# Kernel tuning notes

Measured on AMD Instinct MI355X. Metric: run time of the kernel, lower is better.

Reference implementation:

```python
import jax, jax.numpy as jnp
import numpy as np


def build_perm(total_channels, num_filters):
    """Replicates Net.permuted_new_perfect's nested slice-copies as one gather index."""
    ncpf = total_channels // num_filters
    tg = num_filters + ncpf * ((num_filters - 1) * num_filters) // 2
    perm = np.zeros(tg * ncpf, dtype=np.int32)
    count = 0
    for i in range(num_filters):
        for j in range(ncpf):
            if j == 0:
                for k in range(i, num_filters):
                    perm[count] = i * ncpf
                    perm[count + 1:count + ncpf] = np.arange(k * ncpf + 1, k * ncpf + ncpf)
                    count += ncpf
            else:
                for k in range(i + 1, num_filters):
                    perm[count + j] = i * ncpf + j
                    perm[count:count + j] = np.arange(k * ncpf, k * ncpf + j)
                    perm[count + j + 1:count + ncpf] = np.arange(k * ncpf + j + 1, k * ncpf + ncpf)
                    count += ncpf
    return jnp.asarray(perm)


PERM1 = build_perm(18, 6)    # 153 gathered channels, 51 groups of 3
PERM2 = build_perm(255, 5)   # 26265 gathered channels, 515 groups of 51


def dw_conv(x, w, b, groups):
    y = jax.lax.conv_general_dilated(
        x, w, window_strides=(1, 1), padding='VALID',
        dimension_numbers=('NCHW', 'OIHW', 'NCHW'),
        feature_group_count=groups)
    return y + b[None, :, None, None]


def maxpool2(x):
    return jax.lax.reduce_window(x, -jnp.inf, jax.lax.max,
                                 (1, 1, 2, 2), (1, 1, 2, 2), 'VALID')


def perm_groupconv(x, perm, w, b):
    # gather channels, then grouped 1x1 conv (each group: ncpf chans -> 1 chan)
    G, ncpf = w.shape
    B, _, H, W = x.shape
    xg = x[:, perm].reshape(B, G, ncpf, H, W)
    return jnp.einsum('bgchw,gc->bghw', xg, w) + b[None, :, None, None]


def setup_inputs() -> dict:
    key = jax.random.key(0)
    ks = jax.random.split(key, 17)
    s = 0.05
    return {
        'x': jax.random.normal(ks[0], (64, 3, 32, 32), jnp.float32),
        'dw1_w': jax.random.normal(ks[1], (18, 1, 5, 5), jnp.float32) * s,
        'dw1_b': jax.random.normal(ks[2], (18,), jnp.float32) * s,
        'pc1_w': jax.random.normal(ks[3], (51, 3), jnp.float32) * s,
        'pc1_b': jax.random.normal(ks[4], (51,), jnp.float32) * s,
        'dw2_w': jax.random.normal(ks[5], (255, 1, 5, 5), jnp.float32) * s,
        'dw2_b': jax.random.normal(ks[6], (255,), jnp.float32) * s,
        'pc2_w': jax.random.normal(ks[7], (515, 51), jnp.float32) * s,
        'pc2_b': jax.random.normal(ks[8], (515,), jnp.float32) * s,
        'oo_w': jax.random.normal(ks[9], (100, 515), jnp.float32) * s,
        'oo_b': jax.random.normal(ks[10], (100,), jnp.float32) * s,
        'fc1_w': jax.random.normal(ks[11], (120, 2500), jnp.float32) * s,
        'fc1_b': jax.random.normal(ks[12], (120,), jnp.float32) * s,
        'fc2_w': jax.random.normal(ks[13], (84, 120), jnp.float32) * s,
        'fc2_b': jax.random.normal(ks[14], (84,), jnp.float32) * s,
        'fc3_w': jax.random.normal(ks[15], (10, 84), jnp.float32) * s,
        'fc3_b': jax.random.normal(ks[16], (10,), jnp.float32) * s,
    }


def reference(x, dw1_w, dw1_b, pc1_w, pc1_b, dw2_w, dw2_b, pc2_w, pc2_b,
              oo_w, oo_b, fc1_w, fc1_b, fc2_w, fc2_b, fc3_w, fc3_b):
    h = dw_conv(x, dw1_w, dw1_b, groups=3)            # [B,18,28,28]
    h = perm_groupconv(h, PERM1, pc1_w, pc1_b)        # [B,51,28,28]
    h = maxpool2(jax.nn.relu(h))                      # [B,51,14,14]
    h = dw_conv(h, dw2_w, dw2_b, groups=51)           # [B,255,10,10]
    h = perm_groupconv(h, PERM2, pc2_w, pc2_b)        # [B,515,10,10]
    h = maxpool2(jax.nn.relu(h))                      # [B,515,5,5]
    h = jax.nn.relu(jnp.einsum('bchw,oc->bohw', h, oo_w) + oo_b[None, :, None, None])  # [B,100,5,5]
    h = h.reshape(h.shape[0], -1)                     # [B,2500]
    h = jax.nn.relu(h @ fc1_w.T + fc1_b)
    h = jax.nn.relu(h @ fc2_w.T + fc2_b)
    return h @ fc3_w.T + fc3_b                        # [B,10]
```

## Files before the change

kernel.cpp:

```cpp
#include <hip/hip_runtime.h>

static constexpr size_t OFF_XT = 0;
static constexpr size_t OFF_H1 = 786432;
static constexpr size_t OFF_H2 = 4399104;
static constexpr size_t OFF_H3 = 6958080;
static constexpr size_t OFF_H4 = 13486080;
static constexpr size_t OFF_H5 = 16782080;
static constexpr size_t OFF_H5B = OFF_H1;
static constexpr size_t OFF_H6 = 17422080;
static constexpr size_t OFF_H7 = 17452800;
static constexpr size_t OFF_M1 = 17474304;
static constexpr size_t OFF_M2 = 17475328;
static constexpr size_t OFF_W2 = 17484032;

struct Meta2 { int g; int special; float wj; int valid; };

__device__ inline void scan_ijk(int F, int ncpf, int g, int& oi, int& oj, int& ok) {
  int cnt = 0;
  for (int i = 0; i < F; ++i)
    for (int j = 0; j < ncpf; ++j) {
      int ks = (j == 0) ? i : i + 1;
      for (int k = ks; k < F; ++k) {
        if (cnt == g) { oi = i; oj = j; ok = k; return; }
        ++cnt;
      }
    }
  oi = 0; oj = 0; ok = 0;
}

__device__ inline float4 f4fma(float4 v, float w, float4 a) {
  a.x = fmaf(v.x, w, a.x); a.y = fmaf(v.y, w, a.y);
  a.z = fmaf(v.z, w, a.z); a.w = fmaf(v.w, w, a.w);
  return a;
}

__global__ void k0_setup(const float* __restrict__ x, const float* __restrict__ pc2_w,
                         float* ws) {
  int bx = blockIdx.x, tid = threadIdx.x;
  if (bx < 96) {
    __shared__ float t[64][33];
    int c = bx >> 5, y = bx & 31;
    for (int r = 0; r < 8; ++r) {
      int b = r * 8 + (tid >> 5), xx = tid & 31;
      t[b][xx] = x[((b * 3 + c) * 32 + y) * 32 + xx];
    }
    __syncthreads();
    float* xT = ws + OFF_XT / 4;
    for (int r = 0; r < 8; ++r) {
      int xx = r * 4 + (tid >> 6), b = tid & 63;
      xT[((c * 32 + y) * 32 + xx) * 64 + b] = t[b][xx];
    }
  } else if (bx == 96) {
    if (tid < 51) {
      int i, j, k; scan_ijk(6, 3, tid, i, j, k);
      int* src1 = (int*)((char*)ws + OFF_M1);
      for (int p = 0; p < 3; ++p)
        src1[tid * 4 + p] = (p == j) ? (i * 3 + j) : (k * 3 + p);
    }
  } else if (bx < 204) {
    int idx = (bx - 97) * 256 + tid;
    if (idx < 536 * 51) {
      int s = idx / 51, p = idx - s * 51;
      int k, base;
      if (s < 8)        { k = 0; base = 0; }
      else if (s < 64)  { k = 1; base = 8; }
      else if (s < 168) { k = 2; base = 64; }
      else if (s < 328) { k = 3; base = 168; }
      else              { k = 4; base = 328; }
      int id2 = s - base;
      int cnt = 51 * k + 1;
      Meta2* m2 = (Meta2*)((char*)ws + OFF_M2);
      float* W2 = (float*)((char*)ws + OFF_W2);
      if (id2 < cnt) {
        int i, j;
        if (id2 <= k) { i = id2; j = 0; }
        else { int t2 = id2 - (k + 1); i = t2 / 50; j = t2 - i * 50 + 1; }
        int off = 205 * i - 51 * ((i * (i - 1)) >> 1);
        int g = (j == 0) ? (off + (k - i))
                         : (off + (5 - i) + (j - 1) * (4 - i) + (k - i - 1));
        W2[s * 51 + p] = (p == j) ? 0.f : pc2_w[g * 51 + p];
        if (p == 0) {
          m2[s].g = g; m2[s].special = i * 51 + j;
          m2[s].wj = pc2_w[g * 51 + j]; m2[s].valid = 1;
        }
      } else {
        W2[s * 51 + p] = 0.f;
        if (p == 0) { m2[s].g = 0; m2[s].special = 0; m2[s].wj = 0.f; m2[s].valid = 0; }
      }
    }
  } else {
    int idx = (bx - 204) * 256 + tid;
    if (idx < 7680) (ws + OFF_H6 / 4)[idx] = 0.f;
  }
}

__global__ void __launch_bounds__(256) k1_dw1(const float* __restrict__ w,
                                              const float* __restrict__ bias, float* ws) {
  const float* xT = ws + OFF_XT / 4;
  float* h1 = ws + OFF_H1 / 4;
  int task = blockIdx.x * 4 + __builtin_amdgcn_readfirstlane(threadIdx.y);
  int l = threadIdx.x;
  int sub = l >> 4, b4 = (l & 15) * 4;
  int o = task / 196, rem = task - o * 196;
  int y = rem / 7, xo = (rem - y * 7) * 4 + sub;
  int c = o / 6;
  float bb = bias[o];
  float4 acc = {bb, bb, bb, bb};
  const float* src = xT + ((c * 32 + y) * 32 + xo) * 64 + b4;
  #pragma unroll
  for (int ky = 0; ky < 5; ++ky)
    #pragma unroll
    for (int kx = 0; kx < 5; ++kx) {
      float4 v = *(const float4*)(src + (ky * 32 + kx) * 64);
      acc = f4fma(v, w[o * 25 + ky * 5 + kx], acc);
    }
  *(float4*)(h1 + ((o * 28 + y) * 28 + xo) * 64 + b4) = acc;
}

__global__ void __launch_bounds__(256) k2_pc1(const float* __restrict__ w,
                                              const float* __restrict__ bias, float* ws) {
  const float* h1 = ws + OFF_H1 / 4;
  const int* src1 = (const int*)((const char*)ws + OFF_M1);
  float* h2 = ws + OFF_H2 / 4;
  int task = blockIdx.x * 4 + __builtin_amdgcn_readfirstlane(threadIdx.y);
  if (task >= 2499) return;
  int l = threadIdx.x;
  int sub = l >> 4, b4 = (l & 15) * 4;
  int g = task / 49, pc = task - g * 49;
  int pp = pc * 4 + sub;
  int py = pp / 14, px = pp - py * 14;
  int s0 = src1[g * 4 + 0], s1 = src1[g * 4 + 1], s2 = src1[g * 4 + 2];
  float w0 = w[g * 3 + 0], w1 = w[g * 3 + 1], w2 = w[g * 3 + 2], bb = bias[g];
  float4 m = {0.f, 0.f, 0.f, 0.f};
  #pragma unroll
  for (int dy = 0; dy < 2; ++dy)
    #pragma unroll
    for (int dx = 0; dx < 2; ++dx) {
      int y = py * 2 + dy, xx = px * 2 + dx;
      float4 a = {bb, bb, bb, bb};
      a = f4fma(*(const float4*)(h1 + ((s0 * 28 + y) * 28 + xx) * 64 + b4), w0, a);
      a = f4fma(*(const float4*)(h1 + ((s1 * 28 + y) * 28 + xx) * 64 + b4), w1, a);
      a = f4fma(*(const float4*)(h1 + ((s2 * 28 + y) * 28 + xx) * 64 + b4), w2, a);
      m.x = fmaxf(m.x, a.x); m.y = fmaxf(m.y, a.y);
      m.z = fmaxf(m.z, a.z); m.w = fmaxf(m.w, a.w);
    }
  *(float4*)(h2 + ((g * 14 + py) * 14 + px) * 64 + b4) = m;
}

__global__ void __launch_bounds__(256) k3_dw2(const float* __restrict__ w,
                                              const float* __restrict__ bias, float* ws) {
  const float* h2 = ws + OFF_H2 / 4;
  float* h3 = ws + OFF_H3 / 4;
  int task = blockIdx.x * 4 + __builtin_amdgcn_readfirstlane(threadIdx.y);
  if (task >= 6375) return;
  int l = threadIdx.x;
  int sub = l >> 4, b4 = (l & 15) * 4;
  int o = task / 25, pc = task - o * 25;
  int p = pc * 4 + sub;
  int y = p / 10, xo = p - y * 10;
  int c = o / 5;
  float bb = bias[o];
  float4 acc = {bb, bb, bb, bb};
  const float* src = h2 + ((c * 14 + y) * 14 + xo) * 64 + b4;
  #pragma unroll
  for (int ky = 0; ky < 5; ++ky)
    #pragma unroll
    for (int kx = 0; kx < 5; ++kx) {
      float4 v = *(const float4*)(src + (ky * 14 + kx) * 64);
      acc = f4fma(v, w[o * 25 + ky * 5 + kx], acc);
    }
  int py = y >> 1, dy = y & 1, px = xo >> 1, dx = xo & 1;
  *(float4*)(h3 + ((o * 25 + py * 5 + px) * 4 + dy * 2 + dx) * 64 + b4) = acc;
}

__global__ void __launch_bounds__(256) k4_pc2(const float* __restrict__ bias, float* ws) {
  const float* h3 = ws + OFF_H3 / 4;
  const float* W2 = (const float*)((const char*)ws + OFF_W2);
  const Meta2* m2 = (const Meta2*)((const char*)ws + OFF_M2);
  float* h4 = ws + OFF_H4 / 4;
  int b = threadIdx.x;
  int wv = __builtin_amdgcn_readfirstlane(threadIdx.y);
  int pyx = blockIdx.x;
  int chunk = blockIdx.y;
  int k;
  if (chunk < 1) k = 0; else if (chunk < 8) k = 1; else if (chunk < 21) k = 2;
  else if (chunk < 41) k = 3; else k = 4;
  int s0 = chunk * 8 + wv * 2;
  float acc[2][4];
  #pragma unroll
  for (int m = 0; m < 2; ++m)
    #pragma unroll
    for (int q = 0; q < 4; ++q) acc[m][q] = 0.f;
  const float* hb = h3 + (size_t)(k * 51 * 100 + pyx * 4) * 64 + b;
  const float* wr0 = W2 + (s0 + 0) * 51;
  const float* wr1 = W2 + (s0 + 1) * 51;
  for (int p = 0; p < 51; ++p) {
    float v0 = hb[p * 6400 + 0];
    float v1 = hb[p * 6400 + 64];
    float v2 = hb[p * 6400 + 128];
    float v3 = hb[p * 6400 + 192];
    float wa = wr0[p], wb = wr1[p];
    acc[0][0] = fmaf(v0, wa, acc[0][0]);
    acc[0][1] = fmaf(v1, wa, acc[0][1]);
    acc[0][2] = fmaf(v2, wa, acc[0][2]);
    acc[0][3] = fmaf(v3, wa, acc[0][3]);
    acc[1][0] = fmaf(v0, wb, acc[1][0]);
    acc[1][1] = fmaf(v1, wb, acc[1][1]);
    acc[1][2] = fmaf(v2, wb, acc[1][2]);
    acc[1][3] = fmaf(v3, wb, acc[1][3]);
  }
  #pragma unroll
  for (int m = 0; m < 2; ++m) {
    Meta2 mm = m2[s0 + m];
    if (!mm.valid) continue;
    const float* hs = h3 + (size_t)(mm.special * 100 + pyx * 4) * 64 + b;
    float bb = bias[mm.g];
    float r0 = fmaf(hs[0],   mm.wj, acc[m][0]) + bb;
    float r1 = fmaf(hs[64],  mm.wj, acc[m][1]) + bb;
    float r2 = fmaf(hs[128], mm.wj, acc[m][2]) + bb;
    float r3 = fmaf(hs[192], mm.wj, acc[m][3]) + bb;
    float r = fmaxf(fmaxf(r0, r1), fmaxf(r2, r3));
    h4[(mm.g * 25 + pyx) * 64 + b] = fmaxf(r, 0.f);
  }
}

__global__ void __launch_bounds__(256) k5_oo(const float* __restrict__ w, float* ws) {
  const float* h4 = ws + OFF_H4 / 4;
  __shared__ float red[4][4][64];
  int lane = threadIdx.x;
  int wv = __builtin_amdgcn_readfirstlane(threadIdx.y);
  int pyx = blockIdx.x, og = blockIdx.y, ks = blockIdx.z;
  int kb = ks ? 258 : 0;
  int kn = ks ? 257 : 258;
  int q = kn >> 2, r = kn & 3;
  int base = __builtin_amdgcn_readfirstlane(kb + wv * q + (wv < r ? wv : r));
  int n = q + (wv < r ? 1 : 0);
  const float* w0 = w + (og * 4 + 0) * 515;
  const float* w1 = w + (og * 4 + 1) * 515;
  const float* w2 = w + (og * 4 + 2) * 515;
  const float* w3 = w + (og * 4 + 3) * 515;
  const float* hp = h4 + pyx * 64 + lane;
  float a0 = 0.f, a1 = 0.f, a2 = 0.f, a3 = 0.f;
  #pragma unroll 4
  for (int i = 0; i < n; ++i) {
    int c = base + i;
    float v = hp[c * 1600];
    a0 = fmaf(v, w0[c], a0);
    a1 = fmaf(v, w1[c], a1);
    a2 = fmaf(v, w2[c], a2);
    a3 = fmaf(v, w3[c], a3);
  }
  red[wv][0][lane] = a0; red[wv][1][lane] = a1;
  red[wv][2][lane] = a2; red[wv][3][lane] = a3;
  __syncthreads();
  if (wv == 0) {
    float* h5p = ws + (ks ? OFF_H5B : OFF_H5) / 4;
    #pragma unroll
    for (int m = 0; m < 4; ++m) {
      float s = red[0][m][lane] + red[1][m][lane] + red[2][m][lane] + red[3][m][lane];
      h5p[((og * 4 + m) * 25 + pyx) * 64 + lane] = s;
    }
  }
}

__global__ void __launch_bounds__(256) k6_fc1(const float* __restrict__ w,
                                              const float* __restrict__ oo_b, float* ws) {
  const float* h5a = ws + OFF_H5 / 4;
  const float* h5b = ws + OFF_H5B / 4;
  float* h6 = ws + OFF_H6 / 4;
  __shared__ float red[4][4][64];
  int lane = threadIdx.x;
  int wv = __builtin_amdgcn_readfirstlane(threadIdx.y);
  int og = blockIdx.x, ks = blockIdx.y;
  int kb = ks * 156 + (ks < 4 ? ks : 4);
  int kn = 156 + (ks < 4 ? 1 : 0);
  int q = kn >> 2, r = kn & 3;
  int base = __builtin_amdgcn_readfirstlane(kb + wv * q + (wv < r ? wv : r));
  int n = q + (wv < r ? 1 : 0);
  const float* w0 = w + (og * 4 + 0) * 2500;
  const float* w1 = w + (og * 4 + 1) * 2500;
  const float* w2 = w + (og * 4 + 2) * 2500;
  const float* w3 = w + (og * 4 + 3) * 2500;
  float a0 = 0.f, a1 = 0.f, a2 = 0.f, a3 = 0.f;
  #pragma unroll 4
  for (int i = 0; i < n; ++i) {
    int k = base + i;
    float v = fmaxf(h5a[k * 64 + lane] + h5b[k * 64 + lane] + oo_b[k / 25], 0.f);
    a0 = fmaf(v, w0[k], a0);
    a1 = fmaf(v, w1[k], a1);
    a2 = fmaf(v, w2[k], a2);
    a3 = fmaf(v, w3[k], a3);
  }
  red[wv][0][lane] = a0; red[wv][1][lane] = a1;
  red[wv][2][lane] = a2; red[wv][3][lane] = a3;
  __syncthreads();
  if (wv == 0) {
    #pragma unroll
    for (int m = 0; m < 4; ++m) {
      float s = red[0][m][lane] + red[1][m][lane] + red[2][m][lane] + red[3][m][lane];
      atomicAdd(&h6[(og * 4 + m) * 64 + lane], s);
    }
  }
}

__global__ void __launch_bounds__(256) k7_fc2(const float* __restrict__ w,
                                              const float* __restrict__ fc1_b,
                                              const float* __restrict__ bias, float* ws) {
  const float* h6 = ws + OFF_H6 / 4;
  float* h7 = ws + OFF_H7 / 4;
  __shared__ float red[4][64];
  int lane = threadIdx.x & 63, wv = threadIdx.x >> 6;
  int o = blockIdx.x;
  float acc = 0.f;
  int i0 = wv * 30;
  #pragma unroll 5
  for (int i = i0; i < i0 + 30; ++i) {
    float v = fmaxf(h6[i * 64 + lane] + fc1_b[i], 0.f);
    acc = fmaf(v, w[o * 120 + i], acc);
  }
  red[wv][lane] = acc;
  __syncthreads();
  if (threadIdx.x < 64) {
    float s = red[0][lane] + red[1][lane] + red[2][lane] + red[3][lane] + bias[o];
    h7[o * 64 + lane] = fmaxf(s, 0.f);
  }
}

__global__ void __launch_bounds__(256) k8_fc3(const float* __restrict__ w,
                                              const float* __restrict__ bias,
                                              float* out, const float* ws) {
  const float* h7 = ws + OFF_H7 / 4;
  __shared__ float red[4][64];
  int lane = threadIdx.x & 63, wv = threadIdx.x >> 6;
  int o = blockIdx.x;
  float acc = 0.f;
  int i0 = wv * 21;
  #pragma unroll 7
  for (int i = i0; i < i0 + 21; ++i)
    acc = fmaf(h7[i * 64 + lane], w[o * 84 + i], acc);
  red[wv][lane] = acc;
  __syncthreads();
  if (threadIdx.x < 64) {
    float s = red[0][lane] + red[1][lane] + red[2][lane] + red[3][lane] + bias[o];
    out[lane * 10 + o] = s;
  }
}

extern "C" void kernel_launch(void* const* d_in, const int* in_sizes, int n_in,
                              void* d_out, int out_size, void* d_ws, size_t ws_size,
                              hipStream_t stream) {
  const float* x     = (const float*)d_in[0];
  const float* dw1_w = (const float*)d_in[1];
  const float* dw1_b = (const float*)d_in[2];
  const float* pc1_w = (const float*)d_in[3];
  const float* pc1_b = (const float*)d_in[4];
  const float* dw2_w = (const float*)d_in[5];
  const float* dw2_b = (const float*)d_in[6];
  const float* pc2_w = (const float*)d_in[7];
  const float* pc2_b = (const float*)d_in[8];
  const float* oo_w  = (const float*)d_in[9];
  const float* oo_b  = (const float*)d_in[10];
  const float* fc1_w = (const float*)d_in[11];
  const float* fc1_b = (const float*)d_in[12];
  const float* fc2_w = (const float*)d_in[13];
  const float* fc2_b = (const float*)d_in[14];
  const float* fc3_w = (const float*)d_in[15];
  const float* fc3_b = (const float*)d_in[16];
  float* ws = (float*)d_ws;
  float* out = (float*)d_out;

  hipLaunchKernelGGL(k0_setup, dim3(234), dim3(256), 0, stream, x, pc2_w, ws);
  hipLaunchKernelGGL(k1_dw1, dim3(882), dim3(64, 4), 0, stream, dw1_w, dw1_b, ws);
  hipLaunchKernelGGL(k2_pc1, dim3(625), dim3(64, 4), 0, stream, pc1_w, pc1_b, ws);
  hipLaunchKernelGGL(k3_dw2, dim3(1594), dim3(64, 4), 0, stream, dw2_w, dw2_b, ws);
  hipLaunchKernelGGL(k4_pc2, dim3(25, 67), dim3(64, 4), 0, stream, pc2_b, ws);
  hipLaunchKernelGGL(k5_oo, dim3(25, 25, 2), dim3(64, 4), 0, stream, oo_w, ws);
  hipLaunchKernelGGL(k6_fc1, dim3(30, 16), dim3(64, 4), 0, stream, fc1_w, oo_b, ws);
  hipLaunchKernelGGL(k7_fc2, dim3(84), dim3(256), 0, stream, fc2_w, fc1_b, fc2_b, ws);
  hipLaunchKernelGGL(k8_fc3, dim3(10), dim3(256), 0, stream, fc3_w, fc3_b, out, ws);
}
```

Measured before the change: 150.2 us.

## Fuse 1x1 conv and three FC layers into one per-sample tail kernel

Replaces the oo, fc1, fc2 and fc3 kernels with a single kernel that runs one block per batch sample. Each block stages its slice of h4 in LDS and computes all remaining layers there. This removes three launches, the h5/h6/h7 round-trips through global memory, the atomics and the zeroing of h6 in setup. The cost is only 64 blocks, one per sample, each re-reading the full oo and fc1 weights serially, so parallelism drops sharply.

```diff
diff --git a/kernel.cpp b/kernel.cpp
--- a/kernel.cpp
+++ b/kernel.cpp
@@ -5,10 +5,6 @@
 static constexpr size_t OFF_H2 = 4399104;
 static constexpr size_t OFF_H3 = 6958080;
 static constexpr size_t OFF_H4 = 13486080;
-static constexpr size_t OFF_H5 = 16782080;
-static constexpr size_t OFF_H5B = OFF_H1;
-static constexpr size_t OFF_H6 = 17422080;
-static constexpr size_t OFF_H7 = 17452800;
 static constexpr size_t OFF_M1 = 17474304;
 static constexpr size_t OFF_M2 = 17475328;
 static constexpr size_t OFF_W2 = 17484032;
@@ -57,7 +53,7 @@
       for (int p = 0; p < 3; ++p)
         src1[tid * 4 + p] = (p == j) ? (i * 3 + j) : (k * 3 + p);
     }
-  } else if (bx < 204) {
+  } else {
     int idx = (bx - 97) * 256 + tid;
     if (idx < 536 * 51) {
       int s = idx / 51, p = idx - s * 51;
@@ -88,9 +84,6 @@
         if (p == 0) { m2[s].g = 0; m2[s].special = 0; m2[s].wj = 0.f; m2[s].valid = 0; }
       }
     }
-  } else {
-    int idx = (bx - 204) * 256 + tid;
-    if (idx < 7680) (ws + OFF_H6 / 4)[idx] = 0.f;
   }
 }
 
@@ -224,125 +217,91 @@
   }
 }
 
-__global__ void __launch_bounds__(256) k5_oo(const float* __restrict__ w, float* ws) {
+static constexpr int TL_H4 = 0;
+static constexpr int TL_OL = 12880;
+static constexpr int TL_H6 = 15380;
+static constexpr int TL_H7 = 15504;
+static constexpr int TL_PART = 0;
+
+__global__ void __launch_bounds__(256) k_tail(const float* __restrict__ oo_w,
+                                              const float* __restrict__ oo_b,
+                                              const float* __restrict__ fc1_w,
+                                              const float* __restrict__ fc1_b,
+                                              const float* __restrict__ fc2_w,
+                                              const float* __restrict__ fc2_b,
+                                              const float* __restrict__ fc3_w,
+                                              const float* __restrict__ fc3_b,
+                                              float* out, const float* ws) {
+  __shared__ float lds[16384];
   const float* h4 = ws + OFF_H4 / 4;
-  __shared__ float red[4][4][64];
-  int lane = threadIdx.x;
-  int wv = __builtin_amdgcn_readfirstlane(threadIdx.y);
-  int pyx = blockIdx.x, og = blockIdx.y, ks = blockIdx.z;
-  int kb = ks ? 258 : 0;
-  int kn = ks ? 257 : 258;
-  int q = kn >> 2, r = kn & 3;
-  int base = __builtin_amdgcn_readfirstlane(kb + wv * q + (wv < r ? wv : r));
-  int n = q + (wv < r ? 1 : 0);
-  const float* w0 = w + (og * 4 + 0) * 515;
-  const float* w1 = w + (og * 4 + 1) * 515;
-  const float* w2 = w + (og * 4 + 2) * 515;
-  const float* w3 = w + (og * 4 + 3) * 515;
-  const float* hp = h4 + pyx * 64 + lane;
-  float a0 = 0.f, a1 = 0.f, a2 = 0.f, a3 = 0.f;
-  #pragma unroll 4
-  for (int i = 0; i < n; ++i) {
-    int c = base + i;
-    float v = hp[c * 1600];
-    a0 = fmaf(v, w0[c], a0);
-    a1 = fmaf(v, w1[c], a1);
-    a2 = fmaf(v, w2[c], a2);
-    a3 = fmaf(v, w3[c], a3);
-  }
-  red[wv][0][lane] = a0; red[wv][1][lane] = a1;
-  red[wv][2][lane] = a2; red[wv][3][lane] = a3;
-  __syncthreads();
-  if (wv == 0) {
-    float* h5p = ws + (ks ? OFF_H5B : OFF_H5) / 4;
-    #pragma unroll
-    for (int m = 0; m < 4; ++m) {
-      float s = red[0][m][lane] + red[1][m][lane] + red[2][m][lane] + red[3][m][lane];
-      h5p[((og * 4 + m) * 25 + pyx) * 64 + lane] = s;
-    }
-  }
-}
-
-__global__ void __launch_bounds__(256) k6_fc1(const float* __restrict__ w,
-                                              const float* __restrict__ oo_b, float* ws) {
-  const float* h5a = ws + OFF_H5 / 4;
-  const float* h5b = ws + OFF_H5B / 4;
-  float* h6 = ws + OFF_H6 / 4;
-  __shared__ float red[4][4][64];
-  int lane = threadIdx.x;
-  int wv = __builtin_amdgcn_readfirstlane(threadIdx.y);
-  int og = blockIdx.x, ks = blockIdx.y;
-  int kb = ks * 156 + (ks < 4 ? ks : 4);
-  int kn = 156 + (ks < 4 ? 1 : 0);
-  int q = kn >> 2, r = kn & 3;
-  int base = __builtin_amdgcn_readfirstlane(kb + wv * q + (wv < r ? wv : r));
-  int n = q + (wv < r ? 1 : 0);
-  const float* w0 = w + (og * 4 + 0) * 2500;
-  const float* w1 = w + (og * 4 + 1) * 2500;
-  const float* w2 = w + (og * 4 + 2) * 2500;
-  const float* w3 = w + (og * 4 + 3) * 2500;
-  float a0 = 0.f, a1 = 0.f, a2 = 0.f, a3 = 0.f;
-  #pragma unroll 4
-  for (int i = 0; i < n; ++i) {
-    int k = base + i;
-    float v = fmaxf(h5a[k * 64 + lane] + h5b[k * 64 + lane] + oo_b[k / 25], 0.f);
-    a0 = fmaf(v, w0[k], a0);
-    a1 = fmaf(v, w1[k], a1);
-    a2 = fmaf(v, w2[k], a2);
-    a3 = fmaf(v, w3[k], a3);
-  }
-  red[wv][0][lane] = a0; red[wv][1][lane] = a1;
-  red[wv][2][lane] = a2; red[wv][3][lane] = a3;
-  __syncthreads();
-  if (wv == 0) {
-    #pragma unroll
-    for (int m = 0; m < 4; ++m) {
-      float s = red[0][m][lane] + red[1][m][lane] + red[2][m][lane] + red[3][m][lane];
-      atomicAdd(&h6[(og * 4 + m) * 64 + lane], s);
-    }
-  }
-}
-
-__global__ void __launch_bounds__(256) k7_fc2(const float* __restrict__ w,
-                                              const float* __restrict__ fc1_b,
-                                              const float* __restrict__ bias, float* ws) {
-  const float* h6 = ws + OFF_H6 / 4;
-  float* h7 = ws + OFF_H7 / 4;
-  __shared__ float red[4][64];
-  int lane = threadIdx.x & 63, wv = threadIdx.x >> 6;
-  int o = blockIdx.x;
-  float acc = 0.f;
-  int i0 = wv * 30;
-  #pragma unroll 5
-  for (int i = i0; i < i0 + 30; ++i) {
-    float v = fmaxf(h6[i * 64 + lane] + fc1_b[i], 0.f);
-    acc = fmaf(v, w[o * 120 + i], acc);
-  }
-  red[wv][lane] = acc;
-  __syncthreads();
-  if (threadIdx.x < 64) {
-    float s = red[0][lane] + red[1][lane] + red[2][lane] + red[3][lane] + bias[o];
-    h7[o * 64 + lane] = fmaxf(s, 0.f);
-  }
-}
-
-__global__ void __launch_bounds__(256) k8_fc3(const float* __restrict__ w,
-                                              const float* __restrict__ bias,
-                                              float* out, const float* ws) {
-  const float* h7 = ws + OFF_H7 / 4;
-  __shared__ float red[4][64];
-  int lane = threadIdx.x & 63, wv = threadIdx.x >> 6;
-  int o = blockIdx.x;
-  float acc = 0.f;
-  int i0 = wv * 21;
-  #pragma unroll 7
-  for (int i = i0; i < i0 + 21; ++i)
-    acc = fmaf(h7[i * 64 + lane], w[o * 84 + i], acc);
-  red[wv][lane] = acc;
-  __syncthreads();
-  if (threadIdx.x < 64) {
-    float s = red[0][lane] + red[1][lane] + red[2][lane] + red[3][lane] + bias[o];
-    out[lane * 10 + o] = s;
+  const int b = blockIdx.x;
+  const int t = threadIdx.x;
+
+  for (int i = t; i < 12875; i += 256)
+    lds[TL_H4 + i] = h4[i * 64 + b];
+  __syncthreads();
+
+  if (t < 250) {
+    int pyx = t % 25, og = t / 25;
+    float acc[10];
+    #pragma unroll
+    for (int j = 0; j < 10; ++j) acc[j] = 0.f;
+    const float* wb = oo_w + og * 10 * 515;
+    for (int c = 0; c < 515; ++c) {
+      float v = lds[TL_H4 + c * 25 + pyx];
+      #pragma unroll
+      for (int j = 0; j < 10; ++j)
+        acc[j] = fmaf(v, wb[j * 515 + c], acc[j]);
+    }
+    #pragma unroll
+    for (int j = 0; j < 10; ++j) {
+      int o = og * 10 + j;
+      lds[TL_OL + o * 25 + pyx] = fmaxf(acc[j] + oo_b[o], 0.f);
+    }
+  }
+  __syncthreads();
+
+  if (t < 240) {
+    int og = t / 20, kc = t % 20;
+    float acc[10];
+    #pragma unroll
+    for (int j = 0; j < 10; ++j) acc[j] = 0.f;
+    int kbase = kc * 125;
+    const float* wb = fc1_w + og * 10 * 2500 + kbase;
+    for (int i = 0; i < 125; ++i) {
+      float v = lds[TL_OL + kbase + i];
+      #pragma unroll
+      for (int j = 0; j < 10; ++j)
+        acc[j] = fmaf(v, wb[j * 2500 + i], acc[j]);
+    }
+    #pragma unroll
+    for (int j = 0; j < 10; ++j)
+      lds[TL_PART + (og * 10 + j) * 20 + kc] = acc[j];
+  }
+  __syncthreads();
+  if (t < 120) {
+    float s = fc1_b[t];
+    #pragma unroll
+    for (int kc = 0; kc < 20; ++kc) s += lds[TL_PART + t * 20 + kc];
+    lds[TL_H6 + t] = fmaxf(s, 0.f);
+  }
+  __syncthreads();
+
+  if (t < 84) {
+    float s = fc2_b[t];
+    #pragma unroll 8
+    for (int i = 0; i < 120; ++i)
+      s = fmaf(lds[TL_H6 + i], fc2_w[t * 120 + i], s);
+    lds[TL_H7 + t] = fmaxf(s, 0.f);
+  }
+  __syncthreads();
+
+  if (t < 10) {
+    float s = fc3_b[t];
+    #pragma unroll 7
+    for (int i = 0; i < 84; ++i)
+      s = fmaf(lds[TL_H7 + i], fc3_w[t * 84 + i], s);
+    out[b * 10 + t] = s;
   }
 }
 
@@ -369,13 +328,11 @@
   float* ws = (float*)d_ws;
   float* out = (float*)d_out;
 
-  hipLaunchKernelGGL(k0_setup, dim3(234), dim3(256), 0, stream, x, pc2_w, ws);
+  hipLaunchKernelGGL(k0_setup, dim3(204), dim3(256), 0, stream, x, pc2_w, ws);
   hipLaunchKernelGGL(k1_dw1, dim3(882), dim3(64, 4), 0, stream, dw1_w, dw1_b, ws);
   hipLaunchKernelGGL(k2_pc1, dim3(625), dim3(64, 4), 0, stream, pc1_w, pc1_b, ws);
   hipLaunchKernelGGL(k3_dw2, dim3(1594), dim3(64, 4), 0, stream, dw2_w, dw2_b, ws);
   hipLaunchKernelGGL(k4_pc2, dim3(25, 67), dim3(64, 4), 0, stream, pc2_b, ws);
-  hipLaunchKernelGGL(k5_oo, dim3(25, 25, 2), dim3(64, 4), 0, stream, oo_w, ws);
-  hipLaunchKernelGGL(k6_fc1, dim3(30, 16), dim3(64, 4), 0, stream, fc1_w, oo_b, ws);
-  hipLaunchKernelGGL(k7_fc2, dim3(84), dim3(256), 0, stream, fc2_w, fc1_b, fc2_b, ws);
-  hipLaunchKernelGGL(k8_fc3, dim3(10), dim3(256), 0, stream, fc3_w, fc3_b, out, ws);
-}
+  hipLaunchKernelGGL(k_tail, dim3(64), dim3(256), 0, stream,
+                     oo_w, oo_b, fc1_w, fc1_b, fc2_w, fc2_b, fc3_w, fc3_b, out, ws);
+}
```

Measured after the change: 472.5 us. 215% more time.

## Fuse fc2 and fc3 into one per-sample kernel; widen pc2 register tile

Applied to the files above, without the earlier changes.

Merges the separate fc2 and fc3 kernels into a single kernel with one block per sample, keeping the 120- and 84-wide activations in shared memory, which removes one launch and the global round-trip of h7. Separately, each wave in pc2 now computes four output groups instead of two, so each loaded activation is reused across more weights, and the grid shrinks to about half with per-wave k/s0 mapping and early exit for padding waves. The trade-off is fewer blocks and more registers in pc2, and poorly coalesced per-thread weight-row reads in the fused FC kernel.

```diff
diff --git a/kernel.cpp b/kernel.cpp
--- a/kernel.cpp
+++ b/kernel.cpp
@@ -8,7 +8,6 @@
 static constexpr size_t OFF_H5 = 16782080;
 static constexpr size_t OFF_H5B = OFF_H1;
 static constexpr size_t OFF_H6 = 17422080;
-static constexpr size_t OFF_H7 = 17452800;
 static constexpr size_t OFF_M1 = 17474304;
 static constexpr size_t OFF_M2 = 17475328;
 static constexpr size_t OFF_W2 = 17484032;
@@ -181,25 +180,30 @@
   int b = threadIdx.x;
   int wv = __builtin_amdgcn_readfirstlane(threadIdx.y);
   int pyx = blockIdx.x;
-  int chunk = blockIdx.y;
-  int k;
-  if (chunk < 1) k = 0; else if (chunk < 8) k = 1; else if (chunk < 21) k = 2;
-  else if (chunk < 41) k = 3; else k = 4;
-  int s0 = chunk * 8 + wv * 2;
-  float acc[2][4];
-  #pragma unroll
-  for (int m = 0; m < 2; ++m)
+  int w = blockIdx.y * 4 + wv;
+  int k, s0;
+  if (w < 2)        { k = 0; s0 = w * 4; }
+  else if (w < 16)  { k = 1; s0 = 8 + (w - 2) * 4; }
+  else if (w < 42)  { k = 2; s0 = 64 + (w - 16) * 4; }
+  else if (w < 82)  { k = 3; s0 = 168 + (w - 42) * 4; }
+  else if (w < 134) { k = 4; s0 = 328 + (w - 82) * 4; }
+  else return;
+  float acc[4][4];
+  #pragma unroll
+  for (int m = 0; m < 4; ++m)
     #pragma unroll
     for (int q = 0; q < 4; ++q) acc[m][q] = 0.f;
-  const float* hb = h3 + (size_t)(k * 51 * 100 + pyx * 4) * 64 + b;
+  const float* hb = h3 + (size_t)(k * 5100 + pyx * 4) * 64 + b;
   const float* wr0 = W2 + (s0 + 0) * 51;
   const float* wr1 = W2 + (s0 + 1) * 51;
+  const float* wr2 = W2 + (s0 + 2) * 51;
+  const float* wr3 = W2 + (s0 + 3) * 51;
   for (int p = 0; p < 51; ++p) {
     float v0 = hb[p * 6400 + 0];
     float v1 = hb[p * 6400 + 64];
     float v2 = hb[p * 6400 + 128];
     float v3 = hb[p * 6400 + 192];
-    float wa = wr0[p], wb = wr1[p];
+    float wa = wr0[p], wb = wr1[p], wc = wr2[p], wd = wr3[p];
     acc[0][0] = fmaf(v0, wa, acc[0][0]);
     acc[0][1] = fmaf(v1, wa, acc[0][1]);
     acc[0][2] = fmaf(v2, wa, acc[0][2]);
@@ -208,9 +212,17 @@
     acc[1][1] = fmaf(v1, wb, acc[1][1]);
     acc[1][2] = fmaf(v2, wb, acc[1][2]);
     acc[1][3] = fmaf(v3, wb, acc[1][3]);
-  }
-  #pragma unroll
-  for (int m = 0; m < 2; ++m) {
+    acc[2][0] = fmaf(v0, wc, acc[2][0]);
+    acc[2][1] = fmaf(v1, wc, acc[2][1]);
+    acc[2][2] = fmaf(v2, wc, acc[2][2]);
+    acc[2][3] = fmaf(v3, wc, acc[2][3]);
+    acc[3][0] = fmaf(v0, wd, acc[3][0]);
+    acc[3][1] = fmaf(v1, wd, acc[3][1]);
+    acc[3][2] = fmaf(v2, wd, acc[3][2]);
+    acc[3][3] = fmaf(v3, wd, acc[3][3]);
+  }
+  #pragma unroll
+  for (int m = 0; m < 4; ++m) {
     Meta2 mm = m2[s0 + m];
     if (!mm.valid) continue;
     const float* hs = h3 + (size_t)(mm.special * 100 + pyx * 4) * 64 + b;
@@ -303,46 +315,36 @@
   }
 }
 
-__global__ void __launch_bounds__(256) k7_fc2(const float* __restrict__ w,
-                                              const float* __restrict__ fc1_b,
-                                              const float* __restrict__ bias, float* ws) {
+__global__ void __launch_bounds__(128) k78_fc23(const float* __restrict__ fc1_b,
+                                                const float* __restrict__ fc2_w,
+                                                const float* __restrict__ fc2_b,
+                                                const float* __restrict__ fc3_w,
+                                                const float* __restrict__ fc3_b,
+                                                float* out, const float* ws) {
+  __shared__ float h6c[120];
+  __shared__ float h7c[84];
   const float* h6 = ws + OFF_H6 / 4;
-  float* h7 = ws + OFF_H7 / 4;
-  __shared__ float red[4][64];
-  int lane = threadIdx.x & 63, wv = threadIdx.x >> 6;
-  int o = blockIdx.x;
-  float acc = 0.f;
-  int i0 = wv * 30;
-  #pragma unroll 5
-  for (int i = i0; i < i0 + 30; ++i) {
-    float v = fmaxf(h6[i * 64 + lane] + fc1_b[i], 0.f);
-    acc = fmaf(v, w[o * 120 + i], acc);
-  }
-  red[wv][lane] = acc;
+  const int b = blockIdx.x;
+  const int t = threadIdx.x;
+
+  if (t < 120) h6c[t] = fmaxf(h6[t * 64 + b] + fc1_b[t], 0.f);
   __syncthreads();
-  if (threadIdx.x < 64) {
-    float s = red[0][lane] + red[1][lane] + red[2][lane] + red[3][lane] + bias[o];
-    h7[o * 64 + lane] = fmaxf(s, 0.f);
-  }
-}
-
-__global__ void __launch_bounds__(256) k8_fc3(const float* __restrict__ w,
-                                              const float* __restrict__ bias,
-                                              float* out, const float* ws) {
-  const float* h7 = ws + OFF_H7 / 4;
-  __shared__ float red[4][64];
-  int lane = threadIdx.x & 63, wv = threadIdx.x >> 6;
-  int o = blockIdx.x;
-  float acc = 0.f;
-  int i0 = wv * 21;
-  #pragma unroll 7
-  for (int i = i0; i < i0 + 21; ++i)
-    acc = fmaf(h7[i * 64 + lane], w[o * 84 + i], acc);
-  red[wv][lane] = acc;
+
+  if (t < 84) {
+    float s = fc2_b[t];
+    #pragma unroll 8
+    for (int i = 0; i < 120; ++i)
+      s = fmaf(h6c[i], fc2_w[t * 120 + i], s);
+    h7c[t] = fmaxf(s, 0.f);
+  }
   __syncthreads();
-  if (threadIdx.x < 64) {
-    float s = red[0][lane] + red[1][lane] + red[2][lane] + red[3][lane] + bias[o];
-    out[lane * 10 + o] = s;
+
+  if (t < 10) {
+    float s = fc3_b[t];
+    #pragma unroll 7
+    for (int i = 0; i < 84; ++i)
+      s = fmaf(h7c[i], fc3_w[t * 84 + i], s);
+    out[b * 10 + t] = s;
   }
 }
 
@@ -373,9 +375,9 @@
   hipLaunchKernelGGL(k1_dw1, dim3(882), dim3(64, 4), 0, stream, dw1_w, dw1_b, ws);
   hipLaunchKernelGGL(k2_pc1, dim3(625), dim3(64, 4), 0, stream, pc1_w, pc1_b, ws);
   hipLaunchKernelGGL(k3_dw2, dim3(1594), dim3(64, 4), 0, stream, dw2_w, dw2_b, ws);
-  hipLaunchKernelGGL(k4_pc2, dim3(25, 67), dim3(64, 4), 0, stream, pc2_b, ws);
+  hipLaunchKernelGGL(k4_pc2, dim3(25, 34), dim3(64, 4), 0, stream, pc2_b, ws);
   hipLaunchKernelGGL(k5_oo, dim3(25, 25, 2), dim3(64, 4), 0, stream, oo_w, ws);
   hipLaunchKernelGGL(k6_fc1, dim3(30, 16), dim3(64, 4), 0, stream, fc1_w, oo_b, ws);
-  hipLaunchKernelGGL(k7_fc2, dim3(84), dim3(256), 0, stream, fc2_w, fc1_b, fc2_b, ws);
-  hipLaunchKernelGGL(k8_fc3, dim3(10), dim3(256), 0, stream, fc3_w, fc3_b, out, ws);
-}
+  hipLaunchKernelGGL(k78_fc23, dim3(64), dim3(128), 0, stream,
+                     fc1_b, fc2_w, fc2_b, fc3_w, fc3_b, out, ws);
+}
```

After: 147.9 us. Within noise of the previous version (-1.5%).
